# Kernel optimization log

Measured on AMD Instinct MI355X. Metric: run time of the kernel, lower is better.

Reference implementation:

```python
import jax, jax.numpy as jnp
import numpy as np

B = 4096
D = 512
TEMPERATURE = 0.07


def setup_inputs() -> dict:
    key = jax.random.key(0)
    k1, k2 = jax.random.split(key)
    logits = jax.random.normal(k1, (B, D), dtype=jnp.float32)
    label = jax.random.normal(k2, (B, D), dtype=jnp.float32)
    return {"logits": logits, "label": label}


def reference(logits, label):
    # concat the two views -> [2B, D]
    feats = jnp.concatenate([logits, label], axis=0)
    n = feats.shape[0]
    b = n // 2
    # L2 normalize along feature dim (F.normalize, eps for safety)
    norm = jnp.maximum(jnp.linalg.norm(feats, axis=1, keepdims=True), 1e-12)
    feats = feats / norm
    # similarity matrix [2B, 2B]
    sim = jnp.matmul(feats, feats.T) / TEMPERATURE
    idx = jnp.arange(n)
    # positive pair of row i is row (i + B) mod 2B
    pos = sim[idx, (idx + b) % n]
    # CrossEntropy with target 0 over [pos, negatives] == masked LSE - pos.
    # Mask out the diagonal (self-similarity), which the torch code removes
    # via the boolean-eye mask before building logits.
    neg_inf = jnp.array(-jnp.inf, dtype=sim.dtype)
    sim_masked = jnp.where(idx[:, None] == idx[None, :], neg_inf, sim)
    lse = jax.nn.logsumexp(sim_masked, axis=1)
    loss = jnp.mean(lse - pos)
    return loss
```

## Files before the change

### kernel.cpp

```cpp
#include <hip/hip_runtime.h>
#include <hip/hip_bf16.h>

#define NROWS 8192
#define BHALF 4096
#define DDIM  512

#define BM 128
#define BK 64
#define KSTEPS (DDIM / BK)
#define NT (NROWS / BM)
#define NTRI (NT * (NT + 1) / 2)
#define CPX (NTRI / 8)

#define FSCALE 3.7796447300922722f

typedef short bf16x8 __attribute__((ext_vector_type(8)));
typedef float f32x4 __attribute__((ext_vector_type(4)));
typedef unsigned short u16x8 __attribute__((ext_vector_type(8)));
typedef __attribute__((address_space(1))) unsigned int gu32;
typedef __attribute__((address_space(3))) unsigned int lu32;

__global__ __launch_bounds__(256) void normalize_kernel(
    const float* __restrict__ logits, const float* __restrict__ label,
    unsigned short* __restrict__ fn, float* __restrict__ rowsum,
    float* __restrict__ out) {
  if (blockIdx.x < 8)
    ((float4*)rowsum)[blockIdx.x * 256 + threadIdx.x] =
        make_float4(0.f, 0.f, 0.f, 0.f);
  if (blockIdx.x == 8 && threadIdx.x == 0) out[0] = 0.f;

  const int w = threadIdx.x >> 6, lane = threadIdx.x & 63;
  const int row = blockIdx.x * 4 + w;
  const float* src = (row < BHALF) ? (logits + (size_t)row * DDIM)
                                   : (label + (size_t)(row - BHALF) * DDIM);
  const float4* s4 = (const float4*)src;
  float4 a = s4[lane * 2 + 0];
  float4 b = s4[lane * 2 + 1];
  float ss = a.x * a.x + a.y * a.y + a.z * a.z + a.w * a.w +
             b.x * b.x + b.y * b.y + b.z * b.z + b.w * b.w;
#pragma unroll
  for (int m = 1; m < 64; m <<= 1) ss += __shfl_xor(ss, m);
  const float inv = FSCALE / fmaxf(sqrtf(ss), 1e-12f);
  const float v[8] = {a.x, a.y, a.z, a.w, b.x, b.y, b.z, b.w};
  u16x8 o;
#pragma unroll
  for (int j = 0; j < 8; ++j) {
    float x = v[j] * inv;
    unsigned u = __float_as_uint(x);
    unsigned r = (u + 0x7fffu + ((u >> 16) & 1u)) >> 16;
    o[j] = (unsigned short)r;
  }
  *(u16x8*)(fn + (size_t)row * DDIM + lane * 8) = o;
}

__global__ __launch_bounds__(256) void simexp_tri_kernel(
    const unsigned short* __restrict__ fn, float* __restrict__ rowsum,
    float* __restrict__ pos) {
  __shared__ unsigned short ldsA[2][BM * BK];
  __shared__ unsigned short ldsB[2][BM * BK];
  __shared__ float lds_rsum[BM];
  __shared__ float lds_csum[BM];

  const int bid0 = (int)blockIdx.x;
  const int bid = (bid0 & 7) * CPX + (bid0 >> 3);
  const int u = (NTRI - 1) - bid;
  int k = (int)((sqrtf(8.f * (float)u + 1.f) - 1.f) * 0.5f);
  while ((k + 1) * (k + 2) / 2 <= u) ++k;
  while (k * (k + 1) / 2 > u) --k;
  const int rm = (NT - 1) - k;
  const int cn = (NT - 1) - (u - k * (k + 1) / 2);
  const int rowBase = rm * BM, colBase = cn * BM;
  const bool diag = (rm == cn);
  const bool posTile = (cn == rm + NT / 2);

  const int tid = threadIdx.x;
  const int w = tid >> 6, lane = tid & 63;
  const int wr = w >> 1, wc = w & 1;
  const int l15 = lane & 15, l4 = lane >> 4;

  if (tid < BM) { lds_rsum[tid] = 0.f; lds_csum[tid] = 0.f; }

  const int r8 = lane >> 3;
  const int sgbyte = ((lane & 7) ^ r8) * 16;

  auto stage = [&](unsigned short* dA, unsigned short* dB, int kk) {
#pragma unroll
    for (int i = 0; i < 4; ++i) {
      const int seg = w * 4 + i;
      const int row = seg * 8 + r8;
      const char* gA =
          (const char*)(fn + (size_t)(rowBase + row) * DDIM + kk) + sgbyte;
      const char* gB =
          (const char*)(fn + (size_t)(colBase + row) * DDIM + kk) + sgbyte;
      __builtin_amdgcn_global_load_lds((gu32*)gA,
                                       (lu32*)((char*)dA + seg * 1024), 16, 0, 0);
      __builtin_amdgcn_global_load_lds((gu32*)gB,
                                       (lu32*)((char*)dB + seg * 1024), 16, 0, 0);
    }
  };

  f32x4 acc[4][4];
#pragma unroll
  for (int m = 0; m < 4; ++m)
#pragma unroll
    for (int n = 0; n < 4; ++n) acc[m][n] = (f32x4){0.f, 0.f, 0.f, 0.f};

  auto compute = [&](const unsigned short* sA, const unsigned short* sB) {
#pragma unroll
    for (int ks = 0; ks < 2; ++ks) {
      bf16x8 af[4], bfr[4];
#pragma unroll
      for (int m = 0; m < 4; ++m) {
        const int r = wr * 64 + m * 16 + l15;
        af[m] = *(const bf16x8*)((const char*)sA + r * 128 +
                                 (((ks * 4 + l4) ^ (r & 7)) << 4));
      }
#pragma unroll
      for (int n = 0; n < 4; ++n) {
        const int r = wc * 64 + n * 16 + l15;
        bfr[n] = *(const bf16x8*)((const char*)sB + r * 128 +
                                  (((ks * 4 + l4) ^ (r & 7)) << 4));
      }
#pragma unroll
      for (int m = 0; m < 4; ++m)
#pragma unroll
        for (int n = 0; n < 4; ++n)
          acc[m][n] = __builtin_amdgcn_mfma_f32_16x16x32_bf16(af[m], bfr[n],
                                                              acc[m][n], 0, 0, 0);
    }
  };

  stage(ldsA[0], ldsB[0], 0);
  __syncthreads();
#pragma unroll
  for (int t = 0; t < KSTEPS; t += 2) {
    if (t + 1 < KSTEPS) stage(ldsA[1], ldsB[1], (t + 1) * BK);
    compute(ldsA[0], ldsB[0]);
    __syncthreads();
    if (t + 2 < KSTEPS) stage(ldsA[0], ldsB[0], (t + 2) * BK);
    compute(ldsA[1], ldsB[1]);
    __syncthreads();
  }

  float rs[4][4];
  float cs[4];
#pragma unroll
  for (int m = 0; m < 4; ++m)
#pragma unroll
    for (int j = 0; j < 4; ++j) rs[m][j] = 0.f;
#pragma unroll
  for (int n = 0; n < 4; ++n) cs[n] = 0.f;

#pragma unroll
  for (int m = 0; m < 4; ++m)
#pragma unroll
    for (int n = 0; n < 4; ++n)
#pragma unroll
      for (int j = 0; j < 4; ++j) {
        const int rl = wr * 64 + m * 16 + l4 * 4 + j;
        const int cl = wc * 64 + n * 16 + l15;
        const float v = acc[m][n][j];
        float e = __expf(v);
        if (diag && rl == cl) e = 0.f;
        rs[m][j] += e;
        cs[n] += e;
        if (posTile && rl == cl) pos[rowBase + rl] = v;
      }

#pragma unroll
  for (int m = 0; m < 4; ++m)
#pragma unroll
    for (int j = 0; j < 4; ++j) {
      float s = rs[m][j];
      s += __shfl_xor(s, 1);
      s += __shfl_xor(s, 2);
      s += __shfl_xor(s, 4);
      s += __shfl_xor(s, 8);
      if (l15 == 0) atomicAdd(&lds_rsum[wr * 64 + m * 16 + l4 * 4 + j], s);
    }
  if (!diag) {
#pragma unroll
    for (int n = 0; n < 4; ++n) {
      float s = cs[n];
      s += __shfl_xor(s, 16);
      s += __shfl_xor(s, 32);
      if (l4 == 0) atomicAdd(&lds_csum[wc * 64 + n * 16 + l15], s);
    }
  }
  __syncthreads();
  if (tid < BM) {
    atomicAdd(&rowsum[rowBase + tid], lds_rsum[tid]);
    if (!diag) atomicAdd(&rowsum[colBase + tid], lds_csum[tid]);
  }
}

__global__ __launch_bounds__(256) void reduce_kernel(
    const float* __restrict__ rowsum, const float* __restrict__ pos,
    float* __restrict__ out) {
  __shared__ float part[4];
  const int i = blockIdx.x * 256 + threadIdx.x;
  float a = __logf(rowsum[i]) - pos[i & (BHALF - 1)];
#pragma unroll
  for (int m = 1; m < 64; m <<= 1) a += __shfl_xor(a, m);
  const int w = threadIdx.x >> 6, lane = threadIdx.x & 63;
  if (lane == 0) part[w] = a;
  __syncthreads();
  if (threadIdx.x == 0)
    atomicAdd(out, (part[0] + part[1] + part[2] + part[3]) * (1.0f / NROWS));
}

extern "C" void kernel_launch(void* const* d_in, const int* in_sizes, int n_in,
                              void* d_out, int out_size, void* d_ws, size_t ws_size,
                              hipStream_t stream) {
  const float* logits = (const float*)d_in[0];
  const float* label = (const float*)d_in[1];
  float* out = (float*)d_out;
  unsigned short* fn = (unsigned short*)d_ws;
  float* rowsum = (float*)((char*)d_ws + (size_t)NROWS * DDIM * 2);
  float* pos = rowsum + NROWS;

  normalize_kernel<<<NROWS / 4, 256, 0, stream>>>(logits, label, fn, rowsum, out);
  simexp_tri_kernel<<<NTRI, 256, 0, stream>>>(fn, rowsum, pos);
  reduce_kernel<<<NROWS / 256, 256, 0, stream>>>(rowsum, pos, out);
}
```

Before: 137.2 us.

## Use 256x256 tiles with 8 waves and a phased, barrier-interleaved LDS pipeline

Tiles grow from 128x128 to 256x256 and the block from 4 to 8 waves, each wave owning a 128x64 output piece. The K loop becomes four phases per step, each interleaving a few global-to-LDS loads for the next buffer with MFMA work. Explicit vmcnt/lgkmcnt waits, scheduling barriers and s_setprio control the overlap. This aims to raise arithmetic intensity and hide load latency, at the cost of 128KB of dynamic LDS (one block per CU), many more barriers, and only 528 triangular tiles, which hurts load balance across CUs.

```diff
diff --git a/kernel.cpp b/kernel.cpp
--- a/kernel.cpp
+++ b/kernel.cpp
@@ -5,9 +5,9 @@
 #define BHALF 4096
 #define DDIM  512
 
-#define BM 128
+#define BM 256
 #define BK 64
-#define KSTEPS (DDIM / BK)
+#define KT (DDIM / BK)
 #define NT (NROWS / BM)
 #define NTRI (NT * (NT + 1) / 2)
 #define CPX (NTRI / 8)
@@ -19,6 +19,20 @@
 typedef unsigned short u16x8 __attribute__((ext_vector_type(8)));
 typedef __attribute__((address_space(1))) unsigned int gu32;
 typedef __attribute__((address_space(3))) unsigned int lu32;
+
+#define MFMA_(a, b, c) __builtin_amdgcn_mfma_f32_16x16x32_bf16(a, b, c, 0, 0, 0)
+#define VMCNT(N) asm volatile("s_waitcnt vmcnt(" #N ")" ::: "memory")
+#define LGKM0                                            \
+  do {                                                   \
+    asm volatile("s_waitcnt lgkmcnt(0)" ::: "memory");   \
+    __builtin_amdgcn_sched_barrier(0);                   \
+  } while (0)
+#define BAR                                              \
+  do {                                                   \
+    __builtin_amdgcn_sched_barrier(0);                   \
+    __builtin_amdgcn_s_barrier();                        \
+    __builtin_amdgcn_sched_barrier(0);                   \
+  } while (0)
 
 __global__ __launch_bounds__(256) void normalize_kernel(
     const float* __restrict__ logits, const float* __restrict__ label,
@@ -53,11 +67,10 @@
   *(u16x8*)(fn + (size_t)row * DDIM + lane * 8) = o;
 }
 
-__global__ __launch_bounds__(256) void simexp_tri_kernel(
+__global__ __launch_bounds__(512) void simexp_tri_kernel(
     const unsigned short* __restrict__ fn, float* __restrict__ rowsum,
     float* __restrict__ pos) {
-  __shared__ unsigned short ldsA[2][BM * BK];
-  __shared__ unsigned short ldsB[2][BM * BK];
+  extern __shared__ char lds[];
   __shared__ float lds_rsum[BM];
   __shared__ float lds_csum[BM];
 
@@ -75,89 +88,130 @@
 
   const int tid = threadIdx.x;
   const int w = tid >> 6, lane = tid & 63;
-  const int wr = w >> 1, wc = w & 1;
+  const int wr = w >> 2, wc = w & 3;
   const int l15 = lane & 15, l4 = lane >> 4;
 
   if (tid < BM) { lds_rsum[tid] = 0.f; lds_csum[tid] = 0.f; }
 
   const int r8 = lane >> 3;
-  const int sgbyte = ((lane & 7) ^ r8) * 16;
-
-  auto stage = [&](unsigned short* dA, unsigned short* dB, int kk) {
-#pragma unroll
-    for (int i = 0; i < 4; ++i) {
-      const int seg = w * 4 + i;
-      const int row = seg * 8 + r8;
-      const char* gA =
-          (const char*)(fn + (size_t)(rowBase + row) * DDIM + kk) + sgbyte;
-      const char* gB =
-          (const char*)(fn + (size_t)(colBase + row) * DDIM + kk) + sgbyte;
-      __builtin_amdgcn_global_load_lds((gu32*)gA,
-                                       (lu32*)((char*)dA + seg * 1024), 16, 0, 0);
-      __builtin_amdgcn_global_load_lds((gu32*)gB,
-                                       (lu32*)((char*)dB + seg * 1024), 16, 0, 0);
-    }
-  };
-
-  f32x4 acc[4][4];
-#pragma unroll
-  for (int m = 0; m < 4; ++m)
+  const int sw16 = ((lane & 7) ^ r8) << 4;
+
+  auto stageA = [&](int d, int kk, int R) {
+    const char* g =
+        (const char*)(fn + (size_t)(rowBase + R + w * 8 + r8) * DDIM + kk) + sw16;
+    __builtin_amdgcn_global_load_lds(
+        (gu32*)g, (lu32*)(lds + d * 65536 + (R + w * 8) * 128), 16, 0, 0);
+  };
+  auto stageB = [&](int d, int kk, int R) {
+    const char* g =
+        (const char*)(fn + (size_t)(colBase + R + w * 8 + r8) * DDIM + kk) + sw16;
+    __builtin_amdgcn_global_load_lds(
+        (gu32*)g, (lu32*)(lds + d * 65536 + 32768 + (R + w * 8) * 128), 16, 0, 0);
+  };
+  auto readA = [&](int d, int m, int ks) -> bf16x8 {
+    const int r = wr * 128 + m * 16 + l15;
+    return *(const bf16x8*)(lds + d * 65536 + r * 128 +
+                            (((ks * 4 + l4) ^ (r & 7)) << 4));
+  };
+  auto readB = [&](int d, int n, int ks) -> bf16x8 {
+    const int r = wc * 64 + n * 16 + l15;
+    return *(const bf16x8*)(lds + d * 65536 + 32768 + r * 128 +
+                            (((ks * 4 + l4) ^ (r & 7)) << 4));
+  };
+
+  f32x4 acc[8][4];
+#pragma unroll
+  for (int m = 0; m < 8; ++m)
 #pragma unroll
     for (int n = 0; n < 4; ++n) acc[m][n] = (f32x4){0.f, 0.f, 0.f, 0.f};
 
-  auto compute = [&](const unsigned short* sA, const unsigned short* sB) {
-#pragma unroll
-    for (int ks = 0; ks < 2; ++ks) {
-      bf16x8 af[4], bfr[4];
-#pragma unroll
-      for (int m = 0; m < 4; ++m) {
-        const int r = wr * 64 + m * 16 + l15;
-        af[m] = *(const bf16x8*)((const char*)sA + r * 128 +
-                                 (((ks * 4 + l4) ^ (r & 7)) << 4));
-      }
-#pragma unroll
-      for (int n = 0; n < 4; ++n) {
-        const int r = wc * 64 + n * 16 + l15;
-        bfr[n] = *(const bf16x8*)((const char*)sB + r * 128 +
-                                  (((ks * 4 + l4) ^ (r & 7)) << 4));
-      }
-#pragma unroll
-      for (int m = 0; m < 4; ++m)
-#pragma unroll
-        for (int n = 0; n < 4; ++n)
-          acc[m][n] = __builtin_amdgcn_mfma_f32_16x16x32_bf16(af[m], bfr[n],
-                                                              acc[m][n], 0, 0, 0);
-    }
-  };
-
-  stage(ldsA[0], ldsB[0], 0);
-  __syncthreads();
-#pragma unroll
-  for (int t = 0; t < KSTEPS; t += 2) {
-    if (t + 1 < KSTEPS) stage(ldsA[1], ldsB[1], (t + 1) * BK);
-    compute(ldsA[0], ldsB[0]);
-    __syncthreads();
-    if (t + 2 < KSTEPS) stage(ldsA[0], ldsB[0], (t + 2) * BK);
-    compute(ldsA[1], ldsB[1]);
-    __syncthreads();
-  }
-
-  float rs[4][4];
+#define PHASE0(STAGES)                                                    \
+  {                                                                       \
+    _Pragma("unroll") for (int n = 0; n < 4; ++n) {                       \
+      bf[n][0] = readB(d, n, 0);                                          \
+      bf[n][1] = readB(d, n, 1);                                          \
+    }                                                                     \
+    bf16x8 a00 = readA(d, 0, 0), a01 = readA(d, 0, 1);                    \
+    bf16x8 a10 = readA(d, 1, 0), a11 = readA(d, 1, 1);                    \
+    STAGES;                                                               \
+    BAR;                                                                  \
+    LGKM0;                                                                \
+    __builtin_amdgcn_s_setprio(1);                                        \
+    _Pragma("unroll") for (int n = 0; n < 4; ++n) {                       \
+      acc[0][n] = MFMA_(a00, bf[n][0], acc[0][n]);                        \
+      acc[1][n] = MFMA_(a10, bf[n][0], acc[1][n]);                        \
+    }                                                                     \
+    _Pragma("unroll") for (int n = 0; n < 4; ++n) {                       \
+      acc[0][n] = MFMA_(a01, bf[n][1], acc[0][n]);                        \
+      acc[1][n] = MFMA_(a11, bf[n][1], acc[1][n]);                        \
+    }                                                                     \
+    __builtin_amdgcn_s_setprio(0);                                        \
+    BAR;                                                                  \
+  }
+
+#define PHASE(P, STAGES, TAILWAIT)                                        \
+  {                                                                       \
+    bf16x8 a00 = readA(d, 2 * (P), 0), a01 = readA(d, 2 * (P), 1);        \
+    bf16x8 a10 = readA(d, 2 * (P) + 1, 0), a11 = readA(d, 2 * (P) + 1, 1);\
+    STAGES;                                                               \
+    BAR;                                                                  \
+    LGKM0;                                                                \
+    __builtin_amdgcn_s_setprio(1);                                        \
+    _Pragma("unroll") for (int n = 0; n < 4; ++n) {                       \
+      acc[2 * (P)][n] = MFMA_(a00, bf[n][0], acc[2 * (P)][n]);            \
+      acc[2 * (P) + 1][n] = MFMA_(a10, bf[n][0], acc[2 * (P) + 1][n]);    \
+    }                                                                     \
+    _Pragma("unroll") for (int n = 0; n < 4; ++n) {                       \
+      acc[2 * (P)][n] = MFMA_(a01, bf[n][1], acc[2 * (P)][n]);            \
+      acc[2 * (P) + 1][n] = MFMA_(a11, bf[n][1], acc[2 * (P) + 1][n]);    \
+    }                                                                     \
+    __builtin_amdgcn_s_setprio(0);                                        \
+    TAILWAIT;                                                             \
+    BAR;                                                                  \
+  }
+
+  stageB(0, 0, 0);  stageB(0, 0, 64); stageB(0, 0, 128); stageB(0, 0, 192);
+  stageA(0, 0, 0);  stageA(0, 0, 128);
+  stageA(0, 0, 64); stageA(0, 0, 192);
+  VMCNT(2);
+  BAR;
+
+  for (int t = 0; t < KT - 1; ++t) {
+    const int d = t & 1, o = d ^ 1;
+    const int kn = (t + 1) * BK;
+    bf16x8 bf[4][2];
+    PHASE0(stageB(o, kn, 0); stageB(o, kn, 64));
+    PHASE(1, stageB(o, kn, 128); stageB(o, kn, 192), VMCNT(4));
+    PHASE(2, stageA(o, kn, 0); stageA(o, kn, 128), (void)0);
+    PHASE(3, stageA(o, kn, 64); stageA(o, kn, 192), VMCNT(2));
+  }
+  {
+    const int d = (KT - 1) & 1;
+    bf16x8 bf[4][2];
+    PHASE0((void)0);
+    PHASE(1, (void)0, VMCNT(0));
+    PHASE(2, (void)0, (void)0);
+    PHASE(3, (void)0, (void)0);
+  }
+#undef PHASE0
+#undef PHASE
+
+  float rs[8][4];
   float cs[4];
 #pragma unroll
-  for (int m = 0; m < 4; ++m)
+  for (int m = 0; m < 8; ++m)
 #pragma unroll
     for (int j = 0; j < 4; ++j) rs[m][j] = 0.f;
 #pragma unroll
   for (int n = 0; n < 4; ++n) cs[n] = 0.f;
 
 #pragma unroll
-  for (int m = 0; m < 4; ++m)
+  for (int m = 0; m < 8; ++m)
 #pragma unroll
     for (int n = 0; n < 4; ++n)
 #pragma unroll
       for (int j = 0; j < 4; ++j) {
-        const int rl = wr * 64 + m * 16 + l4 * 4 + j;
+        const int rl = wr * 128 + m * 16 + l4 * 4 + j;
         const int cl = wc * 64 + n * 16 + l15;
         const float v = acc[m][n][j];
         float e = __expf(v);
@@ -168,7 +222,7 @@
       }
 
 #pragma unroll
-  for (int m = 0; m < 4; ++m)
+  for (int m = 0; m < 8; ++m)
 #pragma unroll
     for (int j = 0; j < 4; ++j) {
       float s = rs[m][j];
@@ -176,7 +230,8 @@
       s += __shfl_xor(s, 2);
       s += __shfl_xor(s, 4);
       s += __shfl_xor(s, 8);
-      if (l15 == 0) atomicAdd(&lds_rsum[wr * 64 + m * 16 + l4 * 4 + j], s);
+      if (l15 == 0)
+        atomicAdd(&lds_rsum[wr * 128 + m * 16 + l4 * 4 + j], s);
     }
   if (!diag) {
 #pragma unroll
@@ -220,6 +275,6 @@
   float* pos = rowsum + NROWS;
 
   normalize_kernel<<<NROWS / 4, 256, 0, stream>>>(logits, label, fn, rowsum, out);
-  simexp_tri_kernel<<<NTRI, 256, 0, stream>>>(fn, rowsum, pos);
+  simexp_tri_kernel<<<NTRI, 512, 2 * 65536, stream>>>(fn, rowsum, pos);
   reduce_kernel<<<NROWS / 256, 256, 0, stream>>>(rowsum, pos, out);
 }
```

New measurement: 129.4 us. 5.7% less time.
